# Optimization experiments

Hardware: AMD Instinct MI355X
Metric: run time of the kernel (lower is better)

The kernel has to match this reference:

```python
import jax, jax.numpy as jnp
import numpy as np

EPS_NORM = 1e-12
RMS_EPS = 1e-5


def _rmsnorm(x, w):
    var = jnp.mean(jnp.square(x), axis=-1, keepdims=True)
    return x * jax.lax.rsqrt(var + RMS_EPS) * w


def setup_inputs() -> dict:
    key = jax.random.key(0)
    B, T, D, H, R, K = 2, 512, 1024, 16, 32, 3
    d = D // H
    ks = jax.random.split(key, 11)
    s = 0.02
    return dict(
        x=jax.random.normal(ks[0], (B, T, D), jnp.float32),
        Wq=jax.random.normal(ks[1], (D, D), jnp.float32) * s,
        Wk=jax.random.normal(ks[2], (D, D), jnp.float32) * s,
        Wv=jax.random.normal(ks[3], (D, D), jnp.float32) * s,
        Wo=jax.random.normal(ks[4], (D, D), jnp.float32) * s,
        wA=jax.random.normal(ks[5], (D, R), jnp.float32) * s,
        wB=jax.random.normal(ks[6], (R, D), jnp.float32) * s,
        conv_w=jax.random.normal(ks[7], (D, K), jnp.float32) * 0.5,
        beta_w=jax.random.normal(ks[8], (D, H), jnp.float32) * s,
        g_w=jax.random.normal(ks[9], (D, H), jnp.float32) * s,
        g_b=jnp.zeros((H,), jnp.float32),
        qnorm_w=jnp.ones((d,), jnp.float32),
        knorm_w=jnp.ones((d,), jnp.float32),
    )


def _path_attention(x, Wq, Wk, Wv, Wo, wA, wB, conv_w, beta_w, g_w, g_b, qnorm_w, knorm_w):
    # PaTH attention: s_ij = q_i^T (H_i ... H_{j+1}) k_j / sqrt(d) + (G_i - G_j),
    # H_t = I - beta_t w_t w_t^T (unit w_t), G = cumsum(logsigmoid(forget gate)).
    B, T, D = x.shape
    d = qnorm_w.shape[0]
    H = D // d
    scale = d ** -0.5

    q = (x @ Wq).reshape(B, T, H, d)
    k = (x @ Wk).reshape(B, T, H, d)
    v = (x @ Wv).reshape(B, T, H, d)

    # low-rank W projection + causal depthwise short conv (size 3) + silu
    w = (x @ wA) @ wB                                      # [B,T,D]
    wp = jnp.pad(w, ((0, 0), (2, 0), (0, 0)))
    w = wp[:, 0:T] * conv_w[:, 0] + wp[:, 1:T + 1] * conv_w[:, 1] + wp[:, 2:T + 2] * conv_w[:, 2]
    w = jax.nn.silu(w).reshape(B, T, H, d)
    # unit Householder directions
    w = w * jax.lax.rsqrt(jnp.sum(jnp.square(w), -1, keepdims=True) + EPS_NORM)

    beta = 2.0 * jax.nn.sigmoid(x @ beta_w)                # [B,T,H], in (0,2)
    g = jax.nn.log_sigmoid(x @ g_w + g_b)                  # [B,T,H] forget gate, log-space

    q = _rmsnorm(q, qnorm_w)
    k = _rmsnorm(k, knorm_w)

    # -> [B,H,T,(d)]
    q, k, v, w = (t.transpose(0, 2, 1, 3) for t in (q, k, v, w))
    beta = beta.transpose(0, 2, 1)
    g = g.transpose(0, 2, 1)

    # UT/WY form: A_{t,j} = w_t . (H_{t-1}...H_{j+1} k_j), t > j, via unit-lower tri solve:
    #   A_{t,j} + sum_{s<t} beta_s (w_t.w_s) A_{s,j} = (w_t.k_j) [t>j]
    tri_s = jnp.tril(jnp.ones((T, T), bool), -1)
    C = jnp.einsum('bhtd,bhsd->bhts', w, w) * beta[:, :, None, :]
    L = jnp.where(tri_s, C, 0.0) + jnp.eye(T, dtype=x.dtype)
    Rhs = jnp.where(tri_s, jnp.einsum('bhtd,bhjd->bhtj', w, k), 0.0)
    A = jax.scipy.linalg.solve_triangular(L, Rhs, lower=True, unit_diagonal=True)

    # s_ij = q_i.k_j - sum_{j<t<=i} (q_i.w_t) beta_t A_{t,j}
    tri = jnp.tril(jnp.ones((T, T), bool))
    qw = jnp.where(tri, jnp.einsum('bhid,bhtd->bhit', q, w), 0.0)
    S = jnp.einsum('bhid,bhjd->bhij', q, k) - jnp.einsum('bhit,bhtj->bhij', qw, beta[..., None] * A)

    G = jnp.cumsum(g, axis=-1)                             # [B,H,T]
    logits = S * scale + (G[..., :, None] - G[..., None, :])
    logits = jnp.where(tri, logits, -1e30)
    P = jax.nn.softmax(logits, axis=-1)
    o = jnp.einsum('bhij,bhjd->bhid', P, v)
    return o.transpose(0, 2, 1, 3).reshape(B, T, D) @ Wo


def reference(x, Wq, Wk, Wv, Wo, wA, wB, conv_w, beta_w, g_w, g_b, qnorm_w, knorm_w):
    return _path_attention(x, Wq, Wk, Wv, Wo, wA, wB, conv_w, beta_w, g_w, g_b, qnorm_w, knorm_w)
```

## Files before the change

kernel.cpp:

```cpp
#include <hip/hip_runtime.h>
#include <hip/hip_bf16.h>
#include <math.h>

#define B_ 2
#define T_ 512
#define D_ 1024
#define H_ 16
#define R_ 32
#define DH 64
#define BT_ (B_*T_)
#define BH_ (B_*H_)

typedef __attribute__((ext_vector_type(8))) short bf16x8;
typedef __attribute__((ext_vector_type(4))) short s16x4;
typedef __attribute__((ext_vector_type(4))) float f32x4;

#define MFMA_BF16(a, b, c) __builtin_amdgcn_mfma_f32_16x16x32_bf16(a, b, c, 0, 0, 0)

static __device__ __forceinline__ short bf16s(float v) {
  __hip_bfloat16 b = __float2bfloat16(v);
  return *reinterpret_cast<short*>(&b);
}
static __device__ __forceinline__ float b2f(__hip_bfloat16 h) { return __bfloat162float(h); }

__constant__ int ATT_IT[12]   = {0,1,2,3,4,4,5,5,6,6,7,7};
__constant__ int ATT_J0[12]   = {0,0,0,0,0,3,0,3,0,4,0,4};
__constant__ int ATT_J1[12]   = {0,1,2,3,2,4,2,5,3,6,3,7};
__constant__ int ATT_PART[12] = {-1,-1,-1,-1,0,1,0,1,0,1,0,1};

__device__ __forceinline__ bf16x8 ldfrag(const __hip_bfloat16 s[][72], int b16, int kb, int fr, int kq) {
  return *(const bf16x8*)&s[b16 * 16 + fr][kb * 32 + kq * 8];
}
__device__ __forceinline__ void stage64(const __hip_bfloat16* __restrict__ g, int ldg,
                                        __hip_bfloat16 s[][72], int tid) {
#pragma unroll
  for (int l = 0; l < 2; ++l) {
    int f = tid + l * 256;
    int r = f >> 3, c = (f & 7) << 3;
    *(int4*)&s[r][c] = *(const int4*)&g[(size_t)r * ldg + c];
  }
}

typedef const __attribute__((address_space(1))) void* as1cv;
typedef __attribute__((address_space(3))) void* as3v;
__device__ __forceinline__ void gl16(const __hip_bfloat16* g, __hip_bfloat16* l) {
  __builtin_amdgcn_global_load_lds((as1cv)g, (as3v)l, 16, 0, 0);
}
__device__ __forceinline__ void stage64s(const __hip_bfloat16* __restrict__ g, int ldg,
                                         __hip_bfloat16* s, int tid) {
#pragma unroll
  for (int i = 0; i < 2; ++i) {
    int chunk = tid + i * 256;
    int r = chunk >> 3, c8 = (chunk & 7) ^ (r & 7);
    gl16(g + (size_t)r * ldg + c8 * 8, s + chunk * 8);
  }
}
__device__ __forceinline__ bf16x8 ldfragS(const __hip_bfloat16* s, int b16, int half, int fr, int kq) {
  int r = b16 * 16 + fr;
  int col8 = ((kq + half * 4) ^ (r & 7)) * 8;
  return *(const bf16x8*)&s[r * 64 + col8];
}

__global__ __launch_bounds__(256) void prep_k(const float* __restrict__ x,
                                              const float* __restrict__ Wq,
                                              const float* __restrict__ Wk,
                                              const float* __restrict__ Wv,
                                              const float* __restrict__ Wo,
                                              const float* __restrict__ wA,
                                              const float* __restrict__ bw,
                                              const float* __restrict__ gw,
                                              __hip_bfloat16* __restrict__ xhi,
                                              __hip_bfloat16* __restrict__ xlo,
                                              __hip_bfloat16* __restrict__ wqkvT,
                                              __hip_bfloat16* __restrict__ woT,
                                              __hip_bfloat16* __restrict__ wcThi,
                                              __hip_bfloat16* __restrict__ wcTlo) {
  __shared__ float tile[64][65];
  const int bid = blockIdx.x, tid = threadIdx.x;
  if (bid < 512) {
    int i8 = bid * 256 + tid;
    float4 v0 = ((const float4*)x)[i8 * 2];
    float4 v1 = ((const float4*)x)[i8 * 2 + 1];
    float c[8] = {v0.x, v0.y, v0.z, v0.w, v1.x, v1.y, v1.z, v1.w};
    bf16x8 ph, pl;
#pragma unroll
    for (int u = 0; u < 8; ++u) {
      __hip_bfloat16 h = __float2bfloat16(c[u]);
      ph[u] = *reinterpret_cast<short*>(&h);
      pl[u] = bf16s(c[u] - __bfloat162float(h));
    }
    *(bf16x8*)&xhi[(size_t)i8 * 8] = ph;
    *(bf16x8*)&xlo[(size_t)i8 * 8] = pl;
  } else if (bid < 1536) {
    const int zz = (bid - 512) >> 8, idx = (bid - 512) & 255;
    const float* Wm = (zz == 0) ? Wq : (zz == 1) ? Wk : (zz == 2) ? Wv : Wo;
    __hip_bfloat16* thi = (zz < 3) ? (wqkvT + (size_t)zz * 1024 * D_) : woT;
    const int bn = (idx & 15) * 64, bk = (idx >> 4) * 64;
#pragma unroll
    for (int l = 0; l < 4; ++l) {
      int f = tid + l * 256; int r = f >> 4, c = (f & 15) << 2;
      *(float4*)&tile[r][c] = *(const float4*)&Wm[(size_t)(bk + r) * D_ + bn + c];
    }
    __syncthreads();
#pragma unroll
    for (int l = 0; l < 4; ++l) {
      int f = tid + l * 256; int n = f >> 4, k0 = (f & 15) << 2;
      s16x4 ph;
#pragma unroll
      for (int u = 0; u < 4; ++u) ph[u] = bf16s(tile[k0 + u][n]);
      *(s16x4*)&thi[(size_t)(bn + n) * D_ + bk + k0] = ph;
    }
  } else {
    int n = bid - 1536;
    for (int k = tid; k < D_; k += 256) {
      float v;
      if (n < 32) v = wA[(size_t)k * R_ + n];
      else if (n < 48) v = bw[(size_t)k * H_ + (n - 32)];
      else v = gw[(size_t)k * H_ + (n - 48)];
      __hip_bfloat16 h = __float2bfloat16(v);
      wcThi[(size_t)n * D_ + k] = h;
      wcTlo[(size_t)n * D_ + k] = __float2bfloat16(v - __bfloat162float(h));
    }
  }
}

__global__ __launch_bounds__(256) void gemm_qkv_ycat(const __hip_bfloat16* __restrict__ ah,
                                                     const __hip_bfloat16* __restrict__ al,
                                                     const __hip_bfloat16* __restrict__ bT,
                                                     const __hip_bfloat16* __restrict__ wch,
                                                     const __hip_bfloat16* __restrict__ wcl,
                                                     __hip_bfloat16* __restrict__ qb,
                                                     __hip_bfloat16* __restrict__ kb,
                                                     __hip_bfloat16* __restrict__ vhi,
                                                     float* __restrict__ ypart,
                                                     const float* __restrict__ qnw,
                                                     const float* __restrict__ knw) {
  __shared__ __align__(16) char smem[43008];
  const int bx = blockIdx.x, bm = blockIdx.y * 64;
  const int tid = threadIdx.x, w = tid >> 6, lane = tid & 63;
  const int fr = lane & 15, kq = lane >> 4;
  const f32x4 zf = {0.f, 0.f, 0.f, 0.f};
  f32x4 acc[4] = {zf, zf, zf, zf};

  if (bx < 48) {
    __hip_bfloat16* As = (__hip_bfloat16*)smem;
    __hip_bfloat16* Bs = As + 2 * 4096;
    __hip_bfloat16 (*Lt)[72] = (__hip_bfloat16(*)[72])(Bs + 2 * 4096);
    const int bn = bx * 64;
    const __hip_bfloat16* ap = ah + (size_t)bm * D_;
    const __hip_bfloat16* bp = bT + (size_t)bn * D_;
    stage64s(ap, D_, As, tid);
    stage64s(bp, D_, Bs, tid);
    __syncthreads();
    for (int t = 0; t < 16; ++t) {
      const int cur = t & 1;
      if (t < 15) {
        stage64s(ap + (t + 1) * 64, D_, As + (cur ^ 1) * 4096, tid);
        stage64s(bp + (t + 1) * 64, D_, Bs + (cur ^ 1) * 4096, tid);
      }
      bf16x8 a0 = ldfragS(As + cur * 4096, w, 0, fr, kq);
      bf16x8 a1 = ldfragS(As + cur * 4096, w, 1, fr, kq);
#pragma unroll
      for (int n = 0; n < 4; ++n) {
        acc[n] = MFMA_BF16(a0, ldfragS(Bs + cur * 4096, n, 0, fr, kq), acc[n]);
        acc[n] = MFMA_BF16(a1, ldfragS(Bs + cur * 4096, n, 1, fr, kq), acc[n]);
      }
      __syncthreads();
    }
    if (bn < 2048) {
      float rs[4];
#pragma unroll
      for (int reg = 0; reg < 4; ++reg) {
        float s = 0.f;
#pragma unroll
        for (int n = 0; n < 4; ++n) s += acc[n][reg] * acc[n][reg];
#pragma unroll
        for (int mm = 1; mm <= 8; mm <<= 1) s += __shfl_xor(s, mm);
        rs[reg] = rsqrtf(s * (1.f / DH) + 1e-5f);
      }
      const bool isq = (bn < 1024);
      __hip_bfloat16* outp = isq ? qb : kb;
#pragma unroll
      for (int n = 0; n < 4; ++n) {
        int gn = bn + n * 16 + fr;
        int dd = gn & 63, h = (gn & 1023) >> 6;
        float nw = (isq ? qnw : knw)[dd];
#pragma unroll
        for (int reg = 0; reg < 4; ++reg) {
          int gm = bm + w * 16 + kq * 4 + reg;
          int bb = gm >> 9, tt = gm & 511;
          outp[(((size_t)(bb * H_ + h)) * T_ + tt) * DH + dd] =
              __float2bfloat16(acc[n][reg] * rs[reg] * nw);
        }
      }
    } else {
      const int row0 = w * 16 + kq * 4;
#pragma unroll
      for (int n = 0; n < 4; ++n) {
        int dd = n * 16 + fr;
#pragma unroll
        for (int reg = 0; reg < 4; ++reg) Lt[dd][row0 + reg] = __float2bfloat16(acc[n][reg]);
      }
      __syncthreads();
      const int b = bm >> 9, t0 = bm & 511, h = (bn - 2048) >> 6;
      const size_t base = ((size_t)(b * H_ + h)) * DH * T_;
#pragma unroll
      for (int l = 0; l < 2; ++l) {
        int f = tid + l * 256;
        int dd = f >> 3, tq = (f & 7) * 8;
        *(bf16x8*)&vhi[base + (size_t)dd * T_ + t0 + tq] = *(const bf16x8*)&Lt[dd][tq];
      }
    }
  } else {
    __hip_bfloat16 (*Ah)[72] = (__hip_bfloat16(*)[72])smem;
    __hip_bfloat16 (*Al)[72] = (__hip_bfloat16(*)[72])(smem + 9216);
    __hip_bfloat16 (*Bh)[72] = (__hip_bfloat16(*)[72])(smem + 18432);
    __hip_bfloat16 (*Bl)[72] = (__hip_bfloat16(*)[72])(smem + 27648);
    const int z = bx - 48;
    float* C = ypart + (size_t)z * (BT_ * 64);
    for (int k0 = z * 256; k0 < z * 256 + 256; k0 += 64) {
      __syncthreads();
      stage64(ah + (size_t)bm * D_ + k0, D_, Ah, tid);
      stage64(al + (size_t)bm * D_ + k0, D_, Al, tid);
      stage64(wch + k0, D_, Bh, tid);
      stage64(wcl + k0, D_, Bl, tid);
      __syncthreads();
      bf16x8 ah0 = ldfrag(Ah, w, 0, fr, kq), ah1 = ldfrag(Ah, w, 1, fr, kq);
      bf16x8 al0 = ldfrag(Al, w, 0, fr, kq), al1 = ldfrag(Al, w, 1, fr, kq);
#pragma unroll
      for (int nb = 0; nb < 4; ++nb) {
        bf16x8 b0 = ldfrag(Bh, nb, 0, fr, kq), b1 = ldfrag(Bh, nb, 1, fr, kq);
        bf16x8 c0 = ldfrag(Bl, nb, 0, fr, kq), c1 = ldfrag(Bl, nb, 1, fr, kq);
        acc[nb] = MFMA_BF16(ah0, b0, acc[nb]); acc[nb] = MFMA_BF16(ah1, b1, acc[nb]);
        acc[nb] = MFMA_BF16(ah0, c0, acc[nb]); acc[nb] = MFMA_BF16(ah1, c1, acc[nb]);
        acc[nb] = MFMA_BF16(al0, b0, acc[nb]); acc[nb] = MFMA_BF16(al1, b1, acc[nb]);
      }
    }
#pragma unroll
    for (int nb = 0; nb < 4; ++nb) {
      int n = nb * 16 + fr;
#pragma unroll
      for (int reg = 0; reg < 4; ++reg) {
        int m = bm + w * 16 + kq * 4 + reg;
        C[(size_t)m * 64 + n] = acc[nb][reg];
      }
    }
  }
}

__global__ __launch_bounds__(256) void gemm_o(const __hip_bfloat16* __restrict__ ah,
                                              const __hip_bfloat16* __restrict__ bT,
                                              float* __restrict__ C) {
  __shared__ __hip_bfloat16 As[2][64][64];
  __shared__ __hip_bfloat16 Bs[2][64][64];
  const int bm = blockIdx.y * 64, bn = blockIdx.x * 64;
  const int tid = threadIdx.x, w = tid >> 6, lane = tid & 63;
  const int fr = lane & 15, kq = lane >> 4;
  const f32x4 zf = {0.f, 0.f, 0.f, 0.f};
  f32x4 acc[4] = {zf, zf, zf, zf};
  const __hip_bfloat16* ap = ah + (size_t)bm * D_;
  const __hip_bfloat16* bp = bT + (size_t)bn * D_;
  stage64s(ap, D_, &As[0][0][0], tid);
  stage64s(bp, D_, &Bs[0][0][0], tid);
  __syncthreads();
  for (int t = 0; t < 16; ++t) {
    const int cur = t & 1;
    if (t < 15) {
      stage64s(ap + (t + 1) * 64, D_, &As[cur ^ 1][0][0], tid);
      stage64s(bp + (t + 1) * 64, D_, &Bs[cur ^ 1][0][0], tid);
    }
    bf16x8 a0 = ldfragS(&As[cur][0][0], w, 0, fr, kq);
    bf16x8 a1 = ldfragS(&As[cur][0][0], w, 1, fr, kq);
#pragma unroll
    for (int n = 0; n < 4; ++n) {
      acc[n] = MFMA_BF16(a0, ldfragS(&Bs[cur][0][0], n, 0, fr, kq), acc[n]);
      acc[n] = MFMA_BF16(a1, ldfragS(&Bs[cur][0][0], n, 1, fr, kq), acc[n]);
    }
    __syncthreads();
  }
#pragma unroll
  for (int n = 0; n < 4; ++n) {
    int gn = bn + n * 16 + fr;
#pragma unroll
    for (int reg = 0; reg < 4; ++reg) {
      int gm = bm + w * 16 + kq * 4 + reg;
      C[(size_t)gm * D_ + gn] = acc[n][reg];
    }
  }
}

__global__ __launch_bounds__(512) void gate_wdir(const float* __restrict__ ypart,
                                                 const float* __restrict__ gb,
                                                 const float* __restrict__ wB,
                                                 const float* __restrict__ convw,
                                                 float* __restrict__ beta,
                                                 float* __restrict__ G,
                                                 float* __restrict__ wT,
                                                 __hip_bfloat16* __restrict__ wb16) {
  __shared__ float shm[T_];
  const int bid = blockIdx.x, tid = threadIdx.x;
  if (bid < BT_) {
    int bt = bid, b = bt / T_, t = bt - b * T_;
    float* wl = shm;
    if (tid < 3 * R_) {
      int row = tid / R_, r = tid - row * R_;
      int ts = t - row;
      float a = 0.f;
      if (ts >= 0) {
#pragma unroll
        for (int z = 0; z < 4; ++z)
          a += ypart[(size_t)z * (BT_ * 64) + (size_t)(b * T_ + ts) * 64 + r];
      }
      wl[row * R_ + r] = a;
    }
    __syncthreads();
#pragma unroll
    for (int half = 0; half < 2; ++half) {
      int col = tid + half * 512;
      float f0 = 0.f, f1 = 0.f, f2 = 0.f;
      for (int r = 0; r < R_; ++r) {
        float wb = wB[(size_t)r * D_ + col];
        f0 += wl[0 * R_ + r] * wb; f1 += wl[1 * R_ + r] * wb; f2 += wl[2 * R_ + r] * wb;
      }
      float y = f2 * convw[col * 3 + 0] + f1 * convw[col * 3 + 1] + f0 * convw[col * 3 + 2];
      float s = y / (1.f + expf(-y));
      float ss = s * s;
#pragma unroll
      for (int m = 32; m >= 1; m >>= 1) ss += __shfl_xor(ss, m);
      float outv = s * rsqrtf(ss + 1e-12f);
      int h = col >> 6, dd = col & 63;
      size_t o = (((size_t)(b * H_ + h)) * T_ + t) * DH + dd;
      wT[o] = outv;
      wb16[o] = __float2bfloat16(outv);
    }
  } else {
    int bh = bid - BT_, b = bh >> 4, h = bh & 15, t = tid;
    int bt = b * T_ + t;
    float by = 0.f, gy = gb[h];
#pragma unroll
    for (int z = 0; z < 4; ++z) {
      const float* yp = ypart + (size_t)z * (BT_ * 64) + (size_t)bt * 64;
      by += yp[32 + h];
      gy += yp[48 + h];
    }
    beta[(size_t)bh * T_ + t] = 2.f / (1.f + expf(-by));
    shm[t] = fminf(gy, 0.f) - log1pf(expf(-fabsf(gy)));
    __syncthreads();
    for (int off = 1; off < T_; off <<= 1) {
      float v = (t >= off) ? shm[t - off] : 0.f;
      __syncthreads();
      shm[t] += v;
      __syncthreads();
    }
    G[(size_t)bh * T_ + t] = shm[t];
  }
}

__global__ __launch_bounds__(256) void linv_k(const float* __restrict__ wT,
                                              const float* __restrict__ beta,
                                              __hip_bfloat16* __restrict__ linv) {
  __shared__ float Wsh[64][68];
  __shared__ float Csh[64][65];
  __shared__ float Li[64][68];
  __shared__ float bI[64];
  const int I = blockIdx.x, bhx = blockIdx.y;
  const int tid = threadIdx.x;
#pragma unroll
  for (int l = 0; l < 4; ++l) {
    int f = tid + l * 256; int r = f >> 4, c = (f & 15) << 2;
    *(float4*)&Wsh[r][c] = *(const float4*)&wT[((size_t)bhx * T_ + I * 64 + r) * DH + c];
  }
  if (tid < 64) bI[tid] = beta[(size_t)bhx * T_ + I * 64 + tid];
#pragma unroll
  for (int l = 0; l < 16; ++l) {
    int e = tid + l * 256; int r = e >> 6, c = e & 63;
    Li[r][c] = (r == c) ? 1.f : 0.f;
  }
  __syncthreads();
  const int tm = (tid >> 4) << 2, tn = (tid & 15) << 2;
  float cc[4][4] = {};
  for (int dd = 0; dd < 64; ++dd) {
    float a0 = Wsh[tm + 0][dd], a1 = Wsh[tm + 1][dd], a2 = Wsh[tm + 2][dd], a3 = Wsh[tm + 3][dd];
    float b0 = Wsh[tn + 0][dd], b1 = Wsh[tn + 1][dd], b2 = Wsh[tn + 2][dd], b3 = Wsh[tn + 3][dd];
    cc[0][0] += a0 * b0; cc[0][1] += a0 * b1; cc[0][2] += a0 * b2; cc[0][3] += a0 * b3;
    cc[1][0] += a1 * b0; cc[1][1] += a1 * b1; cc[1][2] += a1 * b2; cc[1][3] += a1 * b3;
    cc[2][0] += a2 * b0; cc[2][1] += a2 * b1; cc[2][2] += a2 * b2; cc[2][3] += a2 * b3;
    cc[3][0] += a3 * b0; cc[3][1] += a3 * b1; cc[3][2] += a3 * b2; cc[3][3] += a3 * b3;
  }
#pragma unroll
  for (int ii = 0; ii < 4; ++ii)
#pragma unroll
    for (int jj = 0; jj < 4; ++jj)
      Csh[tm + ii][tn + jj] = (tm + ii > tn + jj) ? cc[ii][jj] * bI[tn + jj] : 0.f;
  __syncthreads();
  const int sL = tid & 63, g = tid >> 6;
  for (int r0 = 0; r0 < 64; r0 += 8) {
    float a[8];
#pragma unroll
    for (int u = 0; u < 8; ++u) a[u] = Li[r0 + u][sL];
    __syncthreads();
#pragma unroll
    for (int u = 1; u < 8; ++u)
#pragma unroll
      for (int s = 0; s < u; ++s) a[u] -= Csh[r0 + u][r0 + s] * a[s];
    if (g == 0) {
#pragma unroll
      for (int u = 1; u < 8; ++u) Li[r0 + u][sL] = a[u];
    }
    for (int r2 = r0 + 8 + g; r2 < 64; r2 += 4) {
      float acc = Li[r2][sL];
#pragma unroll
      for (int u = 0; u < 8; ++u) acc -= Csh[r2][r0 + u] * a[u];
      Li[r2][sL] = acc;
    }
    __syncthreads();
  }
#pragma unroll
  for (int l = 0; l < 4; ++l) {
    int f = tid + l * 256; int r = f >> 4, c0 = (f & 15) << 2;
    s16x4 p;
    p.x = bf16s(Li[r][c0 + 0]); p.y = bf16s(Li[r][c0 + 1]);
    p.z = bf16s(Li[r][c0 + 2]); p.w = bf16s(Li[r][c0 + 3]);
    *(s16x4*)&linv[((size_t)(bhx * 8 + I)) * 4096 + r * 64 + c0] = p;
  }
}

__global__ __launch_bounds__(256) void chain_k(const __hip_bfloat16* __restrict__ kb,
                                               const __hip_bfloat16* __restrict__ wb,
                                               const __hip_bfloat16* __restrict__ linv,
                                               const float* __restrict__ beta,
                                               __hip_bfloat16* __restrict__ abT,
                                               __hip_bfloat16* __restrict__ khat) {
  __shared__ __hip_bfloat16 Kb[64][72];
  __shared__ __hip_bfloat16 Ws[64][72];
  __shared__ __hip_bfloat16 WsT[64][72];
  __shared__ __hip_bfloat16 Ls[64][72];
  __shared__ __hip_bfloat16 Kh[64][72];
  __shared__ __hip_bfloat16 Ps[64][72];
  __shared__ __hip_bfloat16 Xs[64][72];
  __shared__ float bI[64];
  const int ch = blockIdx.x, bhx = blockIdx.y;
  const int tid = threadIdx.x, w = tid >> 6, lane = tid & 63;
  const int fr = lane & 15, kq = lane >> 4;
  const int jr = w * 16 + kq * 4;
  const size_t hb = (size_t)bhx * T_;
  const f32x4 zf = {0.f, 0.f, 0.f, 0.f};

  stage64(kb + (hb + ch * 64) * DH, DH, Kb, tid);
  f32x4 macc[4] = {zf, zf, zf, zf};

  for (int I = ch; I < 8; ++I) {
    __syncthreads();
    stage64(wb + (hb + I * 64) * DH, DH, Ws, tid);
    stage64(linv + ((size_t)(bhx * 8 + I)) * 4096, 64, Ls, tid);
    if (tid < 64) bI[tid] = beta[hb + I * 64 + tid];
#pragma unroll
    for (int nb = 0; nb < 4; ++nb) {
      int d = nb * 16 + fr;
#pragma unroll
      for (int reg = 0; reg < 4; ++reg)
        Kh[jr + reg][d] = __float2bfloat16(b2f(Kb[jr + reg][d]) - macc[nb][reg]);
    }
    __syncthreads();
#pragma unroll
    for (int l = 0; l < 2; ++l) {
      int f = tid + l * 256;
      int r = f >> 3, c = (f & 7) << 3;
      *(int4*)&khat[(((size_t)(bhx * 8 + I)) * T_ + ch * 64 + r) * DH + c] = *(const int4*)&Kh[r][c];
    }
#pragma unroll
    for (int l = 0; l < 16; ++l) {
      int e = tid + l * 256;
      int t = e >> 6, d = e & 63;
      WsT[d][t] = Ws[t][d];
    }
    bf16x8 kh0 = ldfrag(Kh, w, 0, fr, kq), kh1 = ldfrag(Kh, w, 1, fr, kq);
    f32x4 pt[4];
#pragma unroll
    for (int nb = 0; nb < 4; ++nb) {
      pt[nb] = MFMA_BF16(kh0, ldfrag(Ws, nb, 0, fr, kq), zf);
      pt[nb] = MFMA_BF16(kh1, ldfrag(Ws, nb, 1, fr, kq), pt[nb]);
    }
#pragma unroll
    for (int nb = 0; nb < 4; ++nb) {
      int t = nb * 16 + fr;
#pragma unroll
      for (int reg = 0; reg < 4; ++reg) {
        float v = pt[nb][reg];
        if (I == ch && t <= jr + reg) v = 0.f;
        Ps[jr + reg][t] = __float2bfloat16(v);
      }
    }
    __syncthreads();
    bf16x8 la0 = ldfrag(Ls, w, 0, fr, kq), la1 = ldfrag(Ls, w, 1, fr, kq);
    f32x4 av[4];
#pragma unroll
    for (int nb = 0; nb < 4; ++nb) {
      av[nb] = MFMA_BF16(la0, ldfrag(Ps, nb, 0, fr, kq), zf);
      av[nb] = MFMA_BF16(la1, ldfrag(Ps, nb, 1, fr, kq), av[nb]);
    }
#pragma unroll
    for (int nb = 0; nb < 4; ++nb) {
      s16x4 p;
      p.x = bf16s(bI[jr + 0] * av[nb][0]);
      p.y = bf16s(bI[jr + 1] * av[nb][1]);
      p.z = bf16s(bI[jr + 2] * av[nb][2]);
      p.w = bf16s(bI[jr + 3] * av[nb][3]);
      *(s16x4*)&Xs[nb * 16 + fr][jr] = p;
    }
    __syncthreads();
#pragma unroll
    for (int l = 0; l < 2; ++l) {
      int f = tid + l * 256;
      int r = f >> 3, c = (f & 7) << 3;
      *(int4*)&abT[(hb + ch * 64 + r) * T_ + I * 64 + c] = *(const int4*)&Xs[r][c];
    }
    bf16x8 xa0 = ldfrag(Xs, w, 0, fr, kq), xa1 = ldfrag(Xs, w, 1, fr, kq);
#pragma unroll
    for (int nb = 0; nb < 4; ++nb) {
      macc[nb] = MFMA_BF16(xa0, ldfrag(WsT, nb, 0, fr, kq), macc[nb]);
      macc[nb] = MFMA_BF16(xa1, ldfrag(WsT, nb, 1, fr, kq), macc[nb]);
    }
  }
}

__global__ __launch_bounds__(256) void attn_fused(const __hip_bfloat16* __restrict__ qb,
                                                  const __hip_bfloat16* __restrict__ wb,
                                                  const __hip_bfloat16* __restrict__ khat,
                                                  const __hip_bfloat16* __restrict__ abT,
                                                  const __hip_bfloat16* __restrict__ vhi,
                                                  const float* __restrict__ G,
                                                  __hip_bfloat16* __restrict__ ohi,
                                                  float* __restrict__ opart,
                                                  float* __restrict__ mlbuf) {
  __shared__ __hip_bfloat16 Ms[64][72];
  __shared__ __hip_bfloat16 Ks[64][72];
  __shared__ __hip_bfloat16 Cs[64][72];
  __shared__ __hip_bfloat16 Vh[64][72];
  __shared__ __hip_bfloat16 Ps[64][72];
  const int task = blockIdx.x, bh = blockIdx.y;
  const int it = ATT_IT[task], j0 = ATT_J0[task], j1 = ATT_J1[task], part = ATT_PART[task];
  const int b = bh >> 4, h = bh & 15;
  const int tid = threadIdx.x, w = tid >> 6, lane = tid & 63;
  const int fr = lane & 15, kq = lane >> 4;
  const int row0 = w * 16 + kq * 4;
  const size_t hb = (size_t)bh * T_;
  const f32x4 zero = {0.f, 0.f, 0.f, 0.f};

  stage64(qb + (hb + it * 64) * DH, DH, Ks, tid);
  stage64(wb + (hb + it * 64) * DH, DH, Cs, tid);
  __syncthreads();
  const bf16x8 a0 = ldfrag(Ks, w, 0, fr, kq);
  const bf16x8 a1 = ldfrag(Ks, w, 1, fr, kq);
  f32x4 qw[4];
#pragma unroll
  for (int nb = 0; nb < 4; ++nb) {
    qw[nb] = MFMA_BF16(a0, ldfrag(Cs, nb, 0, fr, kq), zero);
    qw[nb] = MFMA_BF16(a1, ldfrag(Cs, nb, 1, fr, kq), qw[nb]);
  }
#pragma unroll
  for (int nb = 0; nb < 4; ++nb) {
    int col = nb * 16 + fr;
#pragma unroll
    for (int reg = 0; reg < 4; ++reg) {
      float v = -qw[nb][reg];
      if (col > row0 + reg) v = 0.f;
      Ms[row0 + reg][col] = __float2bfloat16(v);
    }
  }
  __syncthreads();
  const bf16x8 m0 = ldfrag(Ms, w, 0, fr, kq);
  const bf16x8 m1 = ldfrag(Ms, w, 1, fr, kq);

  float Gi[4];
#pragma unroll
  for (int reg = 0; reg < 4; ++reg) Gi[reg] = G[hb + it * 64 + row0 + reg];
  float mrow[4] = {-3e38f, -3e38f, -3e38f, -3e38f};
  float lrow[4] = {0.f, 0.f, 0.f, 0.f};
  f32x4 acc_o[4] = {zero, zero, zero, zero};
  const __hip_bfloat16* kh = khat + ((size_t)(bh * 8 + it)) * T_ * DH;

  for (int jt = j0; jt <= j1; ++jt) {
    __syncthreads();
    stage64(kh + (size_t)(jt * 64) * DH, DH, Ks, tid);
    stage64(abT + (hb + jt * 64) * T_ + it * 64, T_, Cs, tid);
    stage64(vhi + (size_t)bh * DH * T_ + jt * 64, T_, Vh, tid);
    __syncthreads();
    f32x4 acc[4];
#pragma unroll
    for (int nb = 0; nb < 4; ++nb) {
      acc[nb] = MFMA_BF16(a0, ldfrag(Ks, nb, 0, fr, kq), zero);
      acc[nb] = MFMA_BF16(a1, ldfrag(Ks, nb, 1, fr, kq), acc[nb]);
      acc[nb] = MFMA_BF16(m0, ldfrag(Cs, nb, 0, fr, kq), acc[nb]);
      acc[nb] = MFMA_BF16(m1, ldfrag(Cs, nb, 1, fr, kq), acc[nb]);
    }
    float gj[4];
#pragma unroll
    for (int nb = 0; nb < 4; ++nb) gj[nb] = G[hb + jt * 64 + nb * 16 + fr];
    const bool diag = (jt == it);
    float vv[4][4];
#pragma unroll
    for (int reg = 0; reg < 4; ++reg) {
      float tm = -3e38f;
#pragma unroll
      for (int nb = 0; nb < 4; ++nb) {
        float vx = acc[nb][reg] * 0.125f + Gi[reg] - gj[nb];
        if (diag && (nb * 16 + fr) > row0 + reg) vx = -3e38f;
        vv[nb][reg] = vx;
        tm = fmaxf(tm, vx);
      }
#pragma unroll
      for (int mm = 1; mm <= 8; mm <<= 1) tm = fmaxf(tm, __shfl_xor(tm, mm));
      float mnew = fmaxf(mrow[reg], tm);
      float sc = __expf(mrow[reg] - mnew);
      mrow[reg] = mnew;
      float tsum = 0.f;
#pragma unroll
      for (int nb = 0; nb < 4; ++nb) {
        float p = __expf(vv[nb][reg] - mnew);
        Ps[row0 + reg][nb * 16 + fr] = __float2bfloat16(p);
        tsum += p;
      }
#pragma unroll
      for (int mm = 1; mm <= 8; mm <<= 1) tsum += __shfl_xor(tsum, mm);
      lrow[reg] = lrow[reg] * sc + tsum;
#pragma unroll
      for (int nb = 0; nb < 4; ++nb) acc_o[nb][reg] *= sc;
    }
    __syncthreads();
    const bf16x8 p0 = ldfrag(Ps, w, 0, fr, kq);
    const bf16x8 p1 = ldfrag(Ps, w, 1, fr, kq);
#pragma unroll
    for (int nb = 0; nb < 4; ++nb) {
      acc_o[nb] = MFMA_BF16(p0, ldfrag(Vh, nb, 0, fr, kq), acc_o[nb]);
      acc_o[nb] = MFMA_BF16(p1, ldfrag(Vh, nb, 1, fr, kq), acc_o[nb]);
    }
  }
  if (part < 0) {
#pragma unroll
    for (int reg = 0; reg < 4; ++reg) {
      float inv = 1.f / lrow[reg];
      int i = it * 64 + row0 + reg;
#pragma unroll
      for (int nb = 0; nb < 4; ++nb) {
        int dd = nb * 16 + fr;
        size_t oi = ((size_t)(b * T_ + i)) * D_ + h * 64 + dd;
        ohi[oi] = __float2bfloat16(acc_o[nb][reg] * inv);
      }
    }
  } else {
    const size_t pb = ((size_t)(bh * 4 + (it - 4)) * 2 + part);
    float* Op = opart + pb * 4096;
    float* mlp = mlbuf + pb * 128;
#pragma unroll
    for (int reg = 0; reg < 4; ++reg) {
      int row = row0 + reg;
#pragma unroll
      for (int nb = 0; nb < 4; ++nb) {
        Op[row * 64 + nb * 16 + fr] = acc_o[nb][reg];
      }
      if (fr == 0) {
        mlp[row] = mrow[reg];
        mlp[64 + row] = lrow[reg];
      }
    }
  }
}

__global__ __launch_bounds__(256) void attn_merge(const float* __restrict__ opart,
                                                  const float* __restrict__ mlbuf,
                                                  __hip_bfloat16* __restrict__ ohi) {
  const int idx = blockIdx.x;
  const int bh = idx >> 2, it = (idx & 3) + 4;
  const int b = bh >> 4, h = bh & 15;
  const int tid = threadIdx.x;
  const float* O0 = opart + ((size_t)idx * 2 + 0) * 4096;
  const float* O1 = opart + ((size_t)idx * 2 + 1) * 4096;
  const float* ml0 = mlbuf + ((size_t)idx * 2 + 0) * 128;
  const float* ml1 = mlbuf + ((size_t)idx * 2 + 1) * 128;
  const int row = tid >> 2, dd0 = (tid & 3) * 16;
  const float m0 = ml0[row], l0 = ml0[64 + row];
  const float m1 = ml1[row], l1 = ml1[64 + row];
  const float m = fmaxf(m0, m1);
  const float e0 = __expf(m0 - m), e1 = __expf(m1 - m);
  const float inv = 1.f / (l0 * e0 + l1 * e1);
  const int i = it * 64 + row;
  const size_t ob = ((size_t)(b * T_ + i)) * D_ + h * 64;
#pragma unroll
  for (int u = 0; u < 16; ++u) {
    int dd = dd0 + u;
    float v = (O0[row * 64 + dd] * e0 + O1[row * 64 + dd] * e1) * inv;
    ohi[ob + dd] = __float2bfloat16(v);
  }
}

extern "C" void kernel_launch(void* const* d_in, const int* in_sizes, int n_in,
                              void* d_out, int out_size, void* d_ws, size_t ws_size,
                              hipStream_t stream) {
  (void)in_sizes; (void)n_in; (void)out_size; (void)ws_size;
  const float* x     = (const float*)d_in[0];
  const float* Wq    = (const float*)d_in[1];
  const float* Wk    = (const float*)d_in[2];
  const float* Wv    = (const float*)d_in[3];
  const float* Wo    = (const float*)d_in[4];
  const float* wA    = (const float*)d_in[5];
  const float* wB    = (const float*)d_in[6];
  const float* convw = (const float*)d_in[7];
  const float* bw    = (const float*)d_in[8];
  const float* gw    = (const float*)d_in[9];
  const float* gb    = (const float*)d_in[10];
  const float* qnw   = (const float*)d_in[11];
  const float* knw   = (const float*)d_in[12];

  const size_t N1 = (size_t)BT_ * D_;
  const size_t NTT = (size_t)BH_ * T_ * T_;
  float* ws = (float*)d_ws;
  float* wTb   = ws;
  float* ypart = wTb + N1;
  float* beta  = ypart + (size_t)4 * BT_ * 64;
  float* G     = beta + (size_t)BH_ * T_;
  float* opart = G + (size_t)BH_ * T_;
  float* mlbuf = opart + (size_t)BH_ * 4 * 2 * 4096;
  __hip_bfloat16* qb16  = (__hip_bfloat16*)(mlbuf + (size_t)BH_ * 4 * 2 * 128);
  __hip_bfloat16* kb16  = qb16 + N1;
  __hip_bfloat16* wb16  = kb16 + N1;
  __hip_bfloat16* abT   = wb16 + N1;
  __hip_bfloat16* linvb = abT + NTT;
  __hip_bfloat16* xhi   = linvb + (size_t)BH_ * 8 * 4096;
  __hip_bfloat16* xlo   = xhi + N1;
  __hip_bfloat16* obhi  = xlo + N1;
  __hip_bfloat16* woThi = obhi + N1;
  __hip_bfloat16* vhi   = woThi + N1;
  __hip_bfloat16* wcThi = vhi + N1;
  __hip_bfloat16* wcTlo = wcThi + (size_t)64 * D_;
  __hip_bfloat16* khat  = wcTlo + (size_t)64 * D_;
  __hip_bfloat16* wqkvT = khat + (size_t)BH_ * 8 * T_ * DH;

  prep_k<<<1600, 256, 0, stream>>>(x, Wq, Wk, Wv, Wo, wA, bw, gw,
                                   xhi, xlo, wqkvT, woThi, wcThi, wcTlo);
  gemm_qkv_ycat<<<dim3(52, 16), 256, 0, stream>>>(xhi, xlo, wqkvT, wcThi, wcTlo,
                                                  qb16, kb16, vhi, ypart, qnw, knw);
  gate_wdir<<<BT_ + BH_, 512, 0, stream>>>(ypart, gb, wB, convw, beta, G, wTb, wb16);
  linv_k<<<dim3(8, BH_), 256, 0, stream>>>(wTb, beta, linvb);
  chain_k<<<dim3(8, BH_), 256, 0, stream>>>(kb16, wb16, linvb, beta, abT, khat);
  attn_fused<<<dim3(12, BH_), 256, 0, stream>>>(qb16, wb16, khat, abT, vhi, G,
                                                obhi, opart, mlbuf);
  attn_merge<<<128, 256, 0, stream>>>(opart, mlbuf, obhi);
  gemm_o<<<dim3(16, 16), 256, 0, stream>>>(obhi, woThi, (float*)d_out);
}
```

Before: 111.5 us.

## Rebalance attention work split into 15 tasks with up to three partials

Attention query tiles are split across more key-range partitions (15 tasks per head instead of 12, with tiles 6 and 7 split three ways) so per-block work is more even and the grid has more blocks. The merge kernel now combines a variable number of partials per tile using a slot table. The chain kernel's per-iteration barrier is also moved outside the loop. That barrier move looks risky: shared buffers are overwritten at the top of each iteration without a preceding sync, which may introduce a race.

```diff
diff --git a/kernel.cpp b/kernel.cpp
--- a/kernel.cpp
+++ b/kernel.cpp
@@ -23,10 +23,12 @@
 }
 static __device__ __forceinline__ float b2f(__hip_bfloat16 h) { return __bfloat162float(h); }
 
-__constant__ int ATT_IT[12]   = {0,1,2,3,4,4,5,5,6,6,7,7};
-__constant__ int ATT_J0[12]   = {0,0,0,0,0,3,0,3,0,4,0,4};
-__constant__ int ATT_J1[12]   = {0,1,2,3,2,4,2,5,3,6,3,7};
-__constant__ int ATT_PART[12] = {-1,-1,-1,-1,0,1,0,1,0,1,0,1};
+__constant__ int ATT_IT[15]   = {0,1,2, 3,3, 4,4, 5,5, 6,6,6, 7,7,7};
+__constant__ int ATT_J0[15]   = {0,0,0, 0,2, 0,3, 0,3, 0,3,5, 0,3,6};
+__constant__ int ATT_J1[15]   = {0,1,2, 1,3, 2,4, 2,5, 2,4,6, 2,5,7};
+__constant__ int ATT_SLOT[15] = {-1,-1,-1, 0,0, 1,1, 2,2, 3,3,3, 4,4,4};
+__constant__ int ATT_PART[15] = {-1,-1,-1, 0,1, 0,1, 0,1, 0,1,2, 0,1,2};
+__constant__ int MRG_NP[5]    = {2,2,2,3,3};
 
 __device__ __forceinline__ bf16x8 ldfrag(const __hip_bfloat16 s[][72], int b16, int kb, int fr, int kq) {
   return *(const bf16x8*)&s[b16 * 16 + fr][kb * 32 + kq * 8];
@@ -448,9 +450,9 @@
 
   stage64(kb + (hb + ch * 64) * DH, DH, Kb, tid);
   f32x4 macc[4] = {zf, zf, zf, zf};
+  __syncthreads();
 
   for (int I = ch; I < 8; ++I) {
-    __syncthreads();
     stage64(wb + (hb + I * 64) * DH, DH, Ws, tid);
     stage64(linv + ((size_t)(bhx * 8 + I)) * 4096, 64, Ls, tid);
     if (tid < 64) bI[tid] = beta[hb + I * 64 + tid];
@@ -539,7 +541,8 @@
   __shared__ __hip_bfloat16 Vh[64][72];
   __shared__ __hip_bfloat16 Ps[64][72];
   const int task = blockIdx.x, bh = blockIdx.y;
-  const int it = ATT_IT[task], j0 = ATT_J0[task], j1 = ATT_J1[task], part = ATT_PART[task];
+  const int it = ATT_IT[task], j0 = ATT_J0[task], j1 = ATT_J1[task];
+  const int slot = ATT_SLOT[task], part = ATT_PART[task];
   const int b = bh >> 4, h = bh & 15;
   const int tid = threadIdx.x, w = tid >> 6, lane = tid & 63;
   const int fr = lane & 15, kq = lane >> 4;
@@ -649,7 +652,7 @@
       }
     }
   } else {
-    const size_t pb = ((size_t)(bh * 4 + (it - 4)) * 2 + part);
+    const size_t pb = ((size_t)(bh * 5 + slot) * 3 + part);
     float* Op = opart + pb * 4096;
     float* mlp = mlbuf + pb * 128;
 #pragma unroll
@@ -671,26 +674,28 @@
                                                   const float* __restrict__ mlbuf,
                                                   __hip_bfloat16* __restrict__ ohi) {
   const int idx = blockIdx.x;
-  const int bh = idx >> 2, it = (idx & 3) + 4;
+  const int bh = idx / 5, slot = idx % 5, it = slot + 3;
+  const int np = MRG_NP[slot];
   const int b = bh >> 4, h = bh & 15;
   const int tid = threadIdx.x;
-  const float* O0 = opart + ((size_t)idx * 2 + 0) * 4096;
-  const float* O1 = opart + ((size_t)idx * 2 + 1) * 4096;
-  const float* ml0 = mlbuf + ((size_t)idx * 2 + 0) * 128;
-  const float* ml1 = mlbuf + ((size_t)idx * 2 + 1) * 128;
   const int row = tid >> 2, dd0 = (tid & 3) * 16;
-  const float m0 = ml0[row], l0 = ml0[64 + row];
-  const float m1 = ml1[row], l1 = ml1[64 + row];
-  const float m = fmaxf(m0, m1);
-  const float e0 = __expf(m0 - m), e1 = __expf(m1 - m);
-  const float inv = 1.f / (l0 * e0 + l1 * e1);
+  const size_t base = (size_t)idx * 3;
+  float mv = -3e38f;
+  for (int p = 0; p < np; ++p) mv = fmaxf(mv, mlbuf[(base + p) * 128 + row]);
+  float lsum = 0.f, e[3];
+  for (int p = 0; p < np; ++p) {
+    e[p] = __expf(mlbuf[(base + p) * 128 + row] - mv);
+    lsum += mlbuf[(base + p) * 128 + 64 + row] * e[p];
+  }
+  const float inv = 1.f / lsum;
   const int i = it * 64 + row;
   const size_t ob = ((size_t)(b * T_ + i)) * D_ + h * 64;
 #pragma unroll
   for (int u = 0; u < 16; ++u) {
     int dd = dd0 + u;
-    float v = (O0[row * 64 + dd] * e0 + O1[row * 64 + dd] * e1) * inv;
-    ohi[ob + dd] = __float2bfloat16(v);
+    float v = 0.f;
+    for (int p = 0; p < np; ++p) v += opart[(base + p) * 4096 + row * 64 + dd] * e[p];
+    ohi[ob + dd] = __float2bfloat16(v * inv);
   }
 }
 
@@ -720,8 +725,8 @@
   float* beta  = ypart + (size_t)4 * BT_ * 64;
   float* G     = beta + (size_t)BH_ * T_;
   float* opart = G + (size_t)BH_ * T_;
-  float* mlbuf = opart + (size_t)BH_ * 4 * 2 * 4096;
-  __hip_bfloat16* qb16  = (__hip_bfloat16*)(mlbuf + (size_t)BH_ * 4 * 2 * 128);
+  float* mlbuf = opart + (size_t)BH_ * 5 * 3 * 4096;
+  __hip_bfloat16* qb16  = (__hip_bfloat16*)(mlbuf + (size_t)BH_ * 5 * 3 * 128);
   __hip_bfloat16* kb16  = qb16 + N1;
   __hip_bfloat16* wb16  = kb16 + N1;
   __hip_bfloat16* abT   = wb16 + N1;
@@ -743,8 +748,8 @@
   gate_wdir<<<BT_ + BH_, 512, 0, stream>>>(ypart, gb, wB, convw, beta, G, wTb, wb16);
   linv_k<<<dim3(8, BH_), 256, 0, stream>>>(wTb, beta, linvb);
   chain_k<<<dim3(8, BH_), 256, 0, stream>>>(kb16, wb16, linvb, beta, abT, khat);
-  attn_fused<<<dim3(12, BH_), 256, 0, stream>>>(qb16, wb16, khat, abT, vhi, G,
+  attn_fused<<<dim3(15, BH_), 256, 0, stream>>>(qb16, wb16, khat, abT, vhi, G,
                                                 obhi, opart, mlbuf);
-  attn_merge<<<128, 256, 0, stream>>>(opart, mlbuf, obhi);
+  attn_merge<<<160, 256, 0, stream>>>(opart, mlbuf, obhi);
   gemm_o<<<dim3(16, 16), 256, 0, stream>>>(obhi, woThi, (float*)d_out);
 }
```

Result: slower. 119.6 us (+7.2%).
